# Kernel optimization log

Hardware: AMD Instinct MI355X
Metric: run time of the kernel (lower is better)

Reference implementation:

```python
import jax, jax.numpy as jnp
import numpy as np

N_SRC = 20000
N_TAR = 20000
DIM = 3


def setup_inputs() -> dict:
    key = jax.random.key(0)
    k1, k2 = jax.random.split(key)
    src_V = jax.random.normal(k1, (N_SRC, DIM), dtype=jnp.float32)
    tar_V = jax.random.normal(k2, (N_TAR, DIM), dtype=jnp.float32)
    return {"src_V": src_V, "tar_V": tar_V}


def reference(src_V, tar_V):
    # Brute-force 1-NN replacing the CPU cKDTree query.
    # Squared distances: ||t||^2 - 2 t.s^T + ||s||^2  -> [M, N]
    d2 = (
        jnp.sum(tar_V * tar_V, axis=1, keepdims=True)
        - 2.0 * (tar_V @ src_V.T)
        + jnp.sum(src_V * src_V, axis=1)[None, :]
    )
    ii = jnp.argmin(d2, axis=1)          # nearest src index per tar point
    diff = src_V[ii] - tar_V             # gather + residual, [M, 3]
    return 0.5 * jnp.sum(diff * diff)
```

## Files before the change

### kernel.cpp

```cpp
#include <hip/hip_runtime.h>
#include <float.h>

#define N_SRC 20000
#define N_TAR 20000
#define TPB 512
#define SPLITS 16
#define TILES 40
#define TGRP 79
#define FBLOCKS ((N_TAR + 255) / 256)

typedef _Float16 half8 __attribute__((ext_vector_type(8)));
typedef float floatx16 __attribute__((ext_vector_type(16)));

__global__ __launch_bounds__(TPB) void nn_mfma(
    const float* __restrict__ src, const float* __restrict__ tar,
    float* __restrict__ part, float* __restrict__ out)
{
    if (blockIdx.x == 0 && blockIdx.y == 0 && threadIdx.x == 0) out[0] = 0.f;

    __shared__ alignas(16) _Float16 lds[TILES * 32 * 16];

    const int tid  = threadIdx.x;
    const int lane = tid & 63;
    const int col  = lane & 31;
    const int half = (lane >> 5) & 1;
    const int wave = tid >> 6;

    const int sbase = blockIdx.y * (TILES * 32);
    for (int ls = tid; ls < TILES * 32; ls += TPB) {
        const int s = sbase + ls;
        half8 f0 = {0, 0, 0, 0, 0, 0, 0, 0};
        half8 f1 = {0, 0, 0, 0, 0, 0, 0, 0};
        if (s < N_SRC) {
            const float x = src[s * 3 + 0];
            const float y = src[s * 3 + 1];
            const float z = src[s * 3 + 2];
            const _Float16 xh = (_Float16)x, yh = (_Float16)y, zh = (_Float16)z;
            const _Float16 xl = (_Float16)(x - (float)xh);
            const _Float16 yl = (_Float16)(y - (float)yh);
            const _Float16 zl = (_Float16)(z - (float)zh);
            const float nrm = 0.5f * (x * x + y * y + z * z);
            const _Float16 nh = (_Float16)nrm;
            const _Float16 nl = (_Float16)(nrm - (float)nh);
            f0 = (half8){xh, yh, zh, xh, yh, zh, xl, yl};
            f1 = (half8){zl, nh, nl, 0, 0, 0, 0, 0};
        } else {
            f1 = (half8){0, (_Float16)30000.f, 0, 0, 0, 0, 0, 0};
        }
        *(half8*)&lds[ls * 16 + 0] = f0;
        *(half8*)&lds[ls * 16 + 8] = f1;
    }

    const int strip = blockIdx.x * 8 + wave;
    const int t = min(strip * 32 + col, N_TAR - 1);
    const float tx = tar[t * 3 + 0];
    const float ty = tar[t * 3 + 1];
    const float tz = tar[t * 3 + 2];
    const _Float16 txh = (_Float16)tx, tyh = (_Float16)ty, tzh = (_Float16)tz;
    const _Float16 txl = (_Float16)(tx - (float)txh);
    const _Float16 tyl = (_Float16)(ty - (float)tyh);
    const _Float16 tzl = (_Float16)(tz - (float)tzh);
    half8 a;
    if (half == 0)
        a = (half8){-txh, -tyh, -tzh, -txl, -tyl, -tzl, -txh, -tyh};
    else
        a = (half8){-tzh, (_Float16)1.f, (_Float16)1.f, 0, 0, 0, 0, 0};

    __syncthreads();

    floatx16 m;
#pragma unroll
    for (int i = 0; i < 16; ++i) m[i] = FLT_MAX;
    const floatx16 zero = {};
    const int foff = col * 16 + half * 8;
#pragma unroll 2
    for (int tile = 0; tile < TILES; ++tile) {
        const half8 b = *(const half8*)&lds[tile * 512 + foff];
        const floatx16 d = __builtin_amdgcn_mfma_f32_32x32x16_f16(a, b, zero, 0, 0, 0);
#pragma unroll
        for (int i = 0; i < 16; ++i) m[i] = fminf(m[i], d[i]);
    }

#pragma unroll
    for (int i = 0; i < 16; ++i) {
        m[i] = fminf(m[i], __shfl_xor(m[i], 1));
        m[i] = fminf(m[i], __shfl_xor(m[i], 2));
        m[i] = fminf(m[i], __shfl_xor(m[i], 4));
        m[i] = fminf(m[i], __shfl_xor(m[i], 8));
        m[i] = fminf(m[i], __shfl_xor(m[i], 16));
    }
    if (col == 0) {
#pragma unroll
        for (int i = 0; i < 16; ++i) {
            const int row = (i & 3) + 8 * (i >> 2) + 4 * half;
            const int tt = min(strip * 32 + row, N_TAR - 1);
            part[blockIdx.y * N_TAR + tt] = m[i];
        }
    }
}

__global__ __launch_bounds__(256) void nn_finalize(
    const float* __restrict__ tar, const float* __restrict__ part,
    float* __restrict__ out)
{
    const int t = blockIdx.x * 256 + threadIdx.x;
    float contrib = 0.f;
    if (t < N_TAR) {
        float m = FLT_MAX;
#pragma unroll
        for (int c = 0; c < SPLITS; ++c) m = fminf(m, part[c * N_TAR + t]);
        const float tx = tar[t * 3 + 0];
        const float ty = tar[t * 3 + 1];
        const float tz = tar[t * 3 + 2];
        contrib = 0.5f * (tx * tx + ty * ty + tz * tz) + m;
    }
    for (int off = 32; off > 0; off >>= 1)
        contrib += __shfl_down(contrib, off);
    __shared__ float red[4];
    if ((threadIdx.x & 63) == 0) red[threadIdx.x >> 6] = contrib;
    __syncthreads();
    if (threadIdx.x == 0) {
        float s = 0.f;
#pragma unroll
        for (int w = 0; w < 4; ++w) s += red[w];
        atomicAdd(out, s);
    }
}

extern "C" void kernel_launch(void* const* d_in, const int* in_sizes, int n_in,
                              void* d_out, int out_size, void* d_ws, size_t ws_size,
                              hipStream_t stream) {
    const float* src = (const float*)d_in[0];
    const float* tar = (const float*)d_in[1];
    float* out = (float*)d_out;
    float* part = (float*)d_ws;

    dim3 grid1(TGRP, SPLITS);
    nn_mfma<<<grid1, TPB, 0, stream>>>(src, tar, part, out);
    nn_finalize<<<FBLOCKS, 256, 0, stream>>>(tar, part, out);
}
```

Measured before the change: 76.97 us.

## Register-block two target strips per wave and use DPP column reduction

Each wave now processes two 32-row target strips against every LDS source tile, so each B fragment feeds four MFMAs instead of one. The grid is halved, which amortises the per-block LDS fill over twice as many targets. The next tile pair is prefetched from LDS ahead of the MFMAs. The shuffle-based column min-reduction is replaced by DPP quad-perm, mirror and row-broadcast steps, with lane 16 writing the result, and a waves-per-EU hint is added. Costs are higher register pressure and fewer blocks to spread across the CUs.

```diff
diff --git a/kernel.cpp b/kernel.cpp
--- a/kernel.cpp
+++ b/kernel.cpp
@@ -6,19 +6,34 @@
 #define TPB 512
 #define SPLITS 16
 #define TILES 40
-#define TGRP 79
+#define TGRP 40
 #define FBLOCKS ((N_TAR + 255) / 256)
 
 typedef _Float16 half8 __attribute__((ext_vector_type(8)));
 typedef float floatx16 __attribute__((ext_vector_type(16)));
 
-__global__ __launch_bounds__(TPB) void nn_mfma(
+
+#define DPP_MIN(v, ctrl) { \
+    const int _s = __builtin_amdgcn_update_dpp( \
+        __float_as_int(v), __float_as_int(v), (ctrl), 0xf, 0xf, false); \
+    v = fminf(v, __int_as_float(_s)); }
+#define COL_REDUCE(v) { \
+    DPP_MIN(v, 0xB1)   \
+    DPP_MIN(v, 0x4E)   \
+    DPP_MIN(v, 0x141)  \
+    DPP_MIN(v, 0x140)  \
+    DPP_MIN(v, 0x142)  }
+
+__global__
+__attribute__((amdgpu_flat_work_group_size(TPB, TPB)))
+__attribute__((amdgpu_waves_per_eu(4)))
+void nn_mfma(
     const float* __restrict__ src, const float* __restrict__ tar,
     float* __restrict__ part, float* __restrict__ out)
 {
     if (blockIdx.x == 0 && blockIdx.y == 0 && threadIdx.x == 0) out[0] = 0.f;
 
-    __shared__ alignas(16) _Float16 lds[TILES * 32 * 16];
+    __shared__ alignas(16) _Float16 lds[TILES * 512];
 
     const int tid  = threadIdx.x;
     const int lane = tid & 63;
@@ -51,50 +66,65 @@
         *(half8*)&lds[ls * 16 + 8] = f1;
     }
 
-    const int strip = blockIdx.x * 8 + wave;
-    const int t = min(strip * 32 + col, N_TAR - 1);
-    const float tx = tar[t * 3 + 0];
-    const float ty = tar[t * 3 + 1];
-    const float tz = tar[t * 3 + 2];
-    const _Float16 txh = (_Float16)tx, tyh = (_Float16)ty, tzh = (_Float16)tz;
-    const _Float16 txl = (_Float16)(tx - (float)txh);
-    const _Float16 tyl = (_Float16)(ty - (float)tyh);
-    const _Float16 tzl = (_Float16)(tz - (float)tzh);
-    half8 a;
-    if (half == 0)
-        a = (half8){-txh, -tyh, -tzh, -txl, -tyl, -tzl, -txh, -tyh};
-    else
-        a = (half8){-tzh, (_Float16)1.f, (_Float16)1.f, 0, 0, 0, 0, 0};
+    const int strip0 = (blockIdx.x * 8 + wave) * 2;
+    half8 a0, a1;
+#pragma unroll
+    for (int sidx = 0; sidx < 2; ++sidx) {
+        const int t = min((strip0 + sidx) * 32 + col, N_TAR - 1);
+        const float tx = tar[t * 3 + 0];
+        const float ty = tar[t * 3 + 1];
+        const float tz = tar[t * 3 + 2];
+        const _Float16 txh = (_Float16)tx, tyh = (_Float16)ty, tzh = (_Float16)tz;
+        const _Float16 txl = (_Float16)(tx - (float)txh);
+        const _Float16 tyl = (_Float16)(ty - (float)tyh);
+        const _Float16 tzl = (_Float16)(tz - (float)tzh);
+        half8 a;
+        if (half == 0)
+            a = (half8){-txh, -tyh, -tzh, -txl, -tyl, -tzl, -txh, -tyh};
+        else
+            a = (half8){-tzh, (_Float16)1.f, (_Float16)1.f, 0, 0, 0, 0, 0};
+        if (sidx == 0) a0 = a; else a1 = a;
+    }
 
     __syncthreads();
 
-    floatx16 m;
+    floatx16 m0, m1;
 #pragma unroll
-    for (int i = 0; i < 16; ++i) m[i] = FLT_MAX;
+    for (int i = 0; i < 16; ++i) { m0[i] = FLT_MAX; m1[i] = FLT_MAX; }
     const floatx16 zero = {};
     const int foff = col * 16 + half * 8;
+
+    half8 b0 = *(const half8*)&lds[0 * 512 + foff];
+    half8 b1 = *(const half8*)&lds[1 * 512 + foff];
 #pragma unroll 2
-    for (int tile = 0; tile < TILES; ++tile) {
-        const half8 b = *(const half8*)&lds[tile * 512 + foff];
-        const floatx16 d = __builtin_amdgcn_mfma_f32_32x32x16_f16(a, b, zero, 0, 0, 0);
+    for (int tp = 0; tp < TILES; tp += 2) {
+        const int nx = min(tp + 2, TILES - 2);
+        const half8 n0 = *(const half8*)&lds[nx * 512 + foff];
+        const half8 n1 = *(const half8*)&lds[(nx + 1) * 512 + foff];
+        const floatx16 d00 = __builtin_amdgcn_mfma_f32_32x32x16_f16(a0, b0, zero, 0, 0, 0);
+        const floatx16 d01 = __builtin_amdgcn_mfma_f32_32x32x16_f16(a0, b1, zero, 0, 0, 0);
+        const floatx16 d10 = __builtin_amdgcn_mfma_f32_32x32x16_f16(a1, b0, zero, 0, 0, 0);
+        const floatx16 d11 = __builtin_amdgcn_mfma_f32_32x32x16_f16(a1, b1, zero, 0, 0, 0);
 #pragma unroll
-        for (int i = 0; i < 16; ++i) m[i] = fminf(m[i], d[i]);
+        for (int i = 0; i < 16; ++i) {
+            m0[i] = fminf(m0[i], fminf(d00[i], d01[i]));
+            m1[i] = fminf(m1[i], fminf(d10[i], d11[i]));
+        }
+        b0 = n0; b1 = n1;
     }
 
 #pragma unroll
-    for (int i = 0; i < 16; ++i) {
-        m[i] = fminf(m[i], __shfl_xor(m[i], 1));
-        m[i] = fminf(m[i], __shfl_xor(m[i], 2));
-        m[i] = fminf(m[i], __shfl_xor(m[i], 4));
-        m[i] = fminf(m[i], __shfl_xor(m[i], 8));
-        m[i] = fminf(m[i], __shfl_xor(m[i], 16));
-    }
-    if (col == 0) {
+    for (int i = 0; i < 16; ++i) { COL_REDUCE(m0[i]) COL_REDUCE(m1[i]) }
+
+    if (col == 16) {
+        float* prow = part + (size_t)blockIdx.y * N_TAR;
 #pragma unroll
         for (int i = 0; i < 16; ++i) {
             const int row = (i & 3) + 8 * (i >> 2) + 4 * half;
-            const int tt = min(strip * 32 + row, N_TAR - 1);
-            part[blockIdx.y * N_TAR + tt] = m[i];
+            const int t0 = min(strip0 * 32 + row, N_TAR - 1);
+            const int t1 = min((strip0 + 1) * 32 + row, N_TAR - 1);
+            prow[t0] = m0[i];
+            prow[t1] = m1[i];
         }
     }
 }
```

Measured after the change: 103.8 us. 34.9% more time.
